# Optimization experiments

Hardware: AMD Instinct MI355X
Metric: run time of the kernel (lower is better)

## Reference

```python
import jax, jax.numpy as jnp
import numpy as np

INF = 100000000.0
TOPK = 27


def _box_iou(a, b):
    # a: [N,4] (x1,y1,x2,y2), b: [G,4] -> iou [N,G]
    area_a = (a[:, 2] - a[:, 0]) * (a[:, 3] - a[:, 1])
    area_b = (b[:, 2] - b[:, 0]) * (b[:, 3] - b[:, 1])
    lt = jnp.maximum(a[:, None, :2], b[None, :, :2])
    rb = jnp.minimum(a[:, None, 2:], b[None, :, 2:])
    wh = jnp.clip(rb - lt, 0.0)
    inter = wh[..., 0] * wh[..., 1]
    union = area_a[:, None] + area_b[None, :] - inter
    return inter / union, union


def _assign_one(anchors, gts, tokens):
    # anchors [N,4], gts [G,4], tokens [G,T]
    N = anchors.shape[0]
    G = gts.shape[0]
    ious, _ = _box_iou(anchors, gts)  # [N,G]

    a_cx = (anchors[:, 2] + anchors[:, 0]) * 0.5
    a_cy = (anchors[:, 3] + anchors[:, 1]) * 0.5
    g_cx = (gts[:, 2] + gts[:, 0]) * 0.5
    g_cy = (gts[:, 3] + gts[:, 1]) * 0.5

    # pairwise center distance [N,G]
    dist = jnp.sqrt((a_cx[:, None] - g_cx[None, :]) ** 2 +
                    (a_cy[:, None] - g_cy[None, :]) ** 2)

    # topk nearest anchors per gt (smallest distance) -> idxs [G,TOPK]
    _, topk_idxs = jax.lax.top_k(-dist.T, TOPK)

    # candidate ious [G,TOPK]
    cand = jnp.take_along_axis(ious.T, topk_idxs, axis=1)
    iou_mean = cand.mean(axis=1)
    iou_std = cand.std(axis=1, ddof=1)  # torch.std is unbiased
    is_pos = cand >= (iou_mean + iou_std)[:, None]

    # center-inside-gt check [G,TOPK]
    ax = a_cx[topk_idxs]
    ay = a_cy[topk_idxs]
    l = ax - gts[:, 0:1]
    t = ay - gts[:, 1:2]
    r = gts[:, 2:3] - ax
    b = gts[:, 3:4] - ay
    is_in_gts = jnp.minimum(jnp.minimum(l, t), jnp.minimum(r, b)) > 0.01
    is_pos = is_pos & is_in_gts

    # scatter candidate ious into flat [G*N] buffer of -INF (indices are unique)
    flat_idx = (jnp.arange(G)[:, None] * N + topk_idxs).reshape(-1)
    vals = ious.T.reshape(-1)[flat_idx]
    scat = jnp.where(is_pos.reshape(-1), vals, -INF)
    ious_inf = jnp.full((G * N,), -INF, dtype=ious.dtype).at[flat_idx].set(scat)
    ious_inf = ious_inf.reshape(G, N).T  # [N,G]

    anchors_to_gt_values = ious_inf.max(axis=1)          # [N]
    anchors_to_gt_indexs = ious_inf.argmax(axis=1)       # [N]

    matched_gts = gts[anchors_to_gt_indexs]              # [N,4]

    T = tokens.shape[1]
    unmatched = jnp.zeros((T,), tokens.dtype).at[-1].set(1.0)
    token_labels = jnp.where((anchors_to_gt_values == -INF)[:, None],
                             unmatched[None, :],
                             tokens[anchors_to_gt_indexs])  # [N,T]
    return anchors_to_gt_values, anchors_to_gt_indexs, matched_gts, token_labels


def setup_inputs() -> dict:
    key = jax.random.key(0)
    k1, k2, k3, k4, k5 = jax.random.split(key, 5)
    B, N, G, T = 8, 100000, 64, 256
    # anchors: valid x1<x2, y1<y2 boxes on a ~1024px canvas
    a_c = jax.random.uniform(k1, (B, N, 2), jnp.float32, 0.0, 1024.0)
    a_wh = jax.random.uniform(k2, (B, N, 2), jnp.float32, 8.0, 128.0)
    anchor_boxes = jnp.concatenate([a_c - a_wh / 2, a_c + a_wh / 2], axis=-1)
    g_c = jax.random.uniform(k3, (B, G, 2), jnp.float32, 0.0, 1024.0)
    g_wh = jax.random.uniform(k4, (B, G, 2), jnp.float32, 64.0, 512.0)
    gt_boxes = jnp.concatenate([g_c - g_wh / 2, g_c + g_wh / 2], axis=-1)
    token_map = jax.random.uniform(k5, (B, G, T), jnp.float32)
    return {"anchor_boxes": anchor_boxes, "gt_boxes": gt_boxes,
            "token_map": token_map}


def reference(anchor_boxes, gt_boxes, token_map):
    return jax.vmap(_assign_one)(anchor_boxes, gt_boxes, token_map)
```

## Files before the change

### kernel.cpp

```cpp
#include <hip/hip_runtime.h>
#include <cstdint>

constexpr int B = 8, N = 100000, G = 64, T = 256, TOPK = 27;
constexpr int BN = B * N;
constexpr int CAP = 2048;
#define NEG_INF_VAL (-100000000.0f)

__global__ __launch_bounds__(256) void atss_centers_kernel(
    const float* __restrict__ anchors, float2* __restrict__ ctr)
{
#pragma clang fp contract(off)
  int i = blockIdx.x * 256 + threadIdx.x;
  if (i < BN) {
    float4 ab = ((const float4*)anchors)[i];
    ctr[i] = make_float2((ab.z + ab.x) * 0.5f, (ab.w + ab.y) * 0.5f);
  }
}

__global__ __launch_bounds__(256) void atss_assign_kernel(
    const float* __restrict__ anchors,
    const float2* __restrict__ ctr,
    const float* __restrict__ gts,
    unsigned long long* __restrict__ best)
{
#pragma clang fp contract(off)
  __shared__ float s_d[CAP];
  __shared__ int   s_i[CAP];
  __shared__ int   s_cnt;
  __shared__ int   s_sel[TOPK];
  __shared__ float s_iou[TOPK];
  __shared__ int   s_in[TOPK];
  __shared__ float s_thresh;

  const int bg  = blockIdx.x;
  const int b   = bg / G;
  const int g   = bg % G;
  const int tid = threadIdx.x;

  const float4 gbox = ((const float4*)gts)[bg];
  const float g_cx = (gbox.z + gbox.x) * 0.5f;
  const float g_cy = (gbox.w + gbox.y) * 0.5f;

  const float4*  abase = (const float4*)(anchors + (size_t)b * N * 4);
  const float2*  cbase = ctr + (size_t)b * N;

  float thr = 24.0f;
  int M = 0;
  for (int attempt = 0; attempt < 8; ++attempt) {
    if (tid == 0) s_cnt = 0;
    __syncthreads();
    for (int n = tid; n < N; n += 256) {
      float2 c = cbase[n];
      float dx = c.x - g_cx, dy = c.y - g_cy;
      float d = __fsqrt_rn(__fmul_rn(dx, dx) + __fmul_rn(dy, dy));
      if (d < thr) {
        int p = atomicAdd(&s_cnt, 1);
        if (p < CAP) { s_d[p] = d; s_i[p] = n; }
      }
    }
    __syncthreads();
    int cnt = s_cnt;
    __syncthreads();
    if (cnt >= TOPK && cnt <= CAP) { M = cnt; break; }
    thr = (cnt < TOPK) ? thr * 4.0f : thr * 0.5f;
  }

  for (int s = tid; s < M; s += 256) {
    unsigned long long pk_s =
        ((unsigned long long)__float_as_uint(s_d[s]) << 20) |
        (unsigned long long)(unsigned)s_i[s];
    int rank = 0;
    for (int j = 0; j < M; ++j) {
      unsigned long long pk_j =
          ((unsigned long long)__float_as_uint(s_d[j]) << 20) |
          (unsigned long long)(unsigned)s_i[j];
      rank += (pk_j < pk_s) ? 1 : 0;
    }
    if (rank < TOPK) s_sel[rank] = s_i[s];
  }
  __syncthreads();

  if (tid < TOPK) {
    int a = s_sel[tid];
    float4 ab = abase[a];
    float area_a = __fmul_rn(ab.z - ab.x, ab.w - ab.y);
    float area_b = __fmul_rn(gbox.z - gbox.x, gbox.w - gbox.y);
    float ltx = fmaxf(ab.x, gbox.x), lty = fmaxf(ab.y, gbox.y);
    float rbx = fminf(ab.z, gbox.z), rby = fminf(ab.w, gbox.w);
    float w = fmaxf(rbx - ltx, 0.0f), h = fmaxf(rby - lty, 0.0f);
    float inter = __fmul_rn(w, h);
    float uni = (area_a + area_b) - inter;
    s_iou[tid] = inter / uni;
    float acx = (ab.z + ab.x) * 0.5f, acy = (ab.w + ab.y) * 0.5f;
    float l = acx - gbox.x, t = acy - gbox.y;
    float r = gbox.z - acx, bt = gbox.w - acy;
    float mn = fminf(fminf(l, t), fminf(r, bt));
    s_in[tid] = (mn > 0.01f) ? 1 : 0;
  }
  __syncthreads();

  if (tid == 0) {
    float sum = 0.0f;
    for (int k = 0; k < TOPK; ++k) sum += s_iou[k];
    float mean = sum / (float)TOPK;
    float vs = 0.0f;
    for (int k = 0; k < TOPK; ++k) {
      float d = s_iou[k] - mean;
      vs += __fmul_rn(d, d);
    }
    float sd = __fsqrt_rn(vs / (float)(TOPK - 1));
    s_thresh = mean + sd;
  }
  __syncthreads();

  if (tid < TOPK) {
    float iou = s_iou[tid];
    if (s_in[tid] && iou >= s_thresh) {
      unsigned long long pk =
          ((unsigned long long)__float_as_uint(iou) << 32) |
          (unsigned long long)(0xFFFFFFFFu - (unsigned)g);
      atomicMax(&best[(size_t)b * N + s_sel[tid]], pk);
    }
  }
}

__global__ __launch_bounds__(256) void atss_write_kernel(
    const unsigned long long* __restrict__ best,
    const float* __restrict__ gts,
    const float* __restrict__ tokens,
    float* __restrict__ out)
{
  float* __restrict__ out_val = out;
  float* __restrict__ out_idx = out + (size_t)BN;
  float* __restrict__ out_mg  = out + (size_t)2 * BN;
  float* __restrict__ out_tok = out + (size_t)6 * BN;

  __shared__ int s_row[256];

  const int tid = threadIdx.x;
  const int i0  = blockIdx.x * 256;
  const int i   = i0 + tid;

  unsigned long long p = best[i];
  const int b_ = i / N;
  int g = 0;
  float val = NEG_INF_VAL;
  if (p != 0ULL) {
    g   = (int)(0xFFFFFFFFu - (unsigned)(p & 0xFFFFFFFFULL));
    val = __uint_as_float((unsigned)(p >> 32));
  }
  const int row = b_ * G + g;
  s_row[tid] = (p != 0ULL) ? row : -1;

  out_val[i] = val;
  out_idx[i] = (float)g;
  ((float4*)out_mg)[i] = ((const float4*)gts)[row];
  __syncthreads();

  const int lane = tid & 63;
  const int sub  = tid >> 6;
  const float4* tok4 = (const float4*)tokens;
#pragma unroll 4
  for (int s = 0; s < 64; ++s) {
    int a = (s << 2) + sub;
    int r = s_row[a];
    float4 t;
    if (r >= 0) {
      t = tok4[(size_t)r * 64 + lane];
    } else {
      t = make_float4(0.0f, 0.0f, 0.0f, 0.0f);
      if (lane == 63) t.w = 1.0f;
    }
    ((float4*)(out_tok + (size_t)(i0 + a) * T))[lane] = t;
  }
}

extern "C" void kernel_launch(void* const* d_in, const int* in_sizes, int n_in,
                              void* d_out, int out_size, void* d_ws, size_t ws_size,
                              hipStream_t stream) {
  const float* anchors = (const float*)d_in[0];
  const float* gts     = (const float*)d_in[1];
  const float* tokens  = (const float*)d_in[2];
  float* out = (float*)d_out;

  unsigned long long* best = (unsigned long long*)d_ws;
  float2* ctr = (float2*)((char*)d_ws + sizeof(unsigned long long) * (size_t)BN);

  hipMemsetAsync(best, 0, sizeof(unsigned long long) * (size_t)BN, stream);
  atss_centers_kernel<<<(BN + 255) / 256, 256, 0, stream>>>(anchors, ctr);
  atss_assign_kernel<<<B * G, 256, 0, stream>>>(anchors, ctr, gts, best);
  atss_write_kernel<<<BN / 256, 256, 0, stream>>>(best, gts, tokens, out);
}
```

Measured before the change: 960.1 us.

## Zero token output with memset and sparsely write only matched anchors' tokens

The 800K x 256 token output is now cleared with a bulk memset, and the write kernel only writes the trailing 1.0 for unmatched anchors and copies token rows for matched anchors, which are compacted in shared memory. The zeroing of the best array moves into the centers kernel, replacing its separate memset. This aims to cut per-thread store work in the write kernel, since most anchors are unmatched. The full 800 MB buffer is still written once by the memset, so the gain rests on memset bandwidth beating the kernel's store loop, and the scattered single-float writes add some overhead.

```diff
diff --git a/kernel.cpp b/kernel.cpp
--- a/kernel.cpp
+++ b/kernel.cpp
@@ -6,12 +6,14 @@
 constexpr int CAP = 2048;
 #define NEG_INF_VAL (-100000000.0f)
 
-__global__ __launch_bounds__(256) void atss_centers_kernel(
-    const float* __restrict__ anchors, float2* __restrict__ ctr)
+__global__ __launch_bounds__(256) void atss_prep_kernel(
+    const float* __restrict__ anchors, float2* __restrict__ ctr,
+    unsigned long long* __restrict__ best)
 {
 #pragma clang fp contract(off)
   int i = blockIdx.x * 256 + threadIdx.x;
   if (i < BN) {
+    best[i] = 0ULL;
     float4 ab = ((const float4*)anchors)[i];
     ctr[i] = make_float2((ab.z + ab.x) * 0.5f, (ab.w + ab.y) * 0.5f);
   }
@@ -124,7 +126,7 @@
   }
 }
 
-__global__ __launch_bounds__(256) void atss_write_kernel(
+__global__ __launch_bounds__(256) void atss_sparse_write_kernel(
     const unsigned long long* __restrict__ best,
     const float* __restrict__ gts,
     const float* __restrict__ tokens,
@@ -135,11 +137,16 @@
   float* __restrict__ out_mg  = out + (size_t)2 * BN;
   float* __restrict__ out_tok = out + (size_t)6 * BN;
 
-  __shared__ int s_row[256];
+  __shared__ int s_m_anchor[256];
+  __shared__ int s_m_row[256];
+  __shared__ int s_m_cnt;
 
   const int tid = threadIdx.x;
   const int i0  = blockIdx.x * 256;
   const int i   = i0 + tid;
+
+  if (tid == 0) s_m_cnt = 0;
+  __syncthreads();
 
   unsigned long long p = best[i];
   const int b_ = i / N;
@@ -150,28 +157,28 @@
     val = __uint_as_float((unsigned)(p >> 32));
   }
   const int row = b_ * G + g;
-  s_row[tid] = (p != 0ULL) ? row : -1;
 
   out_val[i] = val;
   out_idx[i] = (float)g;
   ((float4*)out_mg)[i] = ((const float4*)gts)[row];
+
+  if (p != 0ULL) {
+    int s = atomicAdd(&s_m_cnt, 1);
+    s_m_anchor[s] = i;
+    s_m_row[s]    = row;
+  } else {
+    out_tok[(size_t)i * T + (T - 1)] = 1.0f;
+  }
   __syncthreads();
 
   const int lane = tid & 63;
-  const int sub  = tid >> 6;
+  const int wv   = tid >> 6;
+  const int cnt  = s_m_cnt;
   const float4* tok4 = (const float4*)tokens;
-#pragma unroll 4
-  for (int s = 0; s < 64; ++s) {
-    int a = (s << 2) + sub;
-    int r = s_row[a];
-    float4 t;
-    if (r >= 0) {
-      t = tok4[(size_t)r * 64 + lane];
-    } else {
-      t = make_float4(0.0f, 0.0f, 0.0f, 0.0f);
-      if (lane == 63) t.w = 1.0f;
-    }
-    ((float4*)(out_tok + (size_t)(i0 + a) * T))[lane] = t;
+  for (int s = wv; s < cnt; s += 4) {
+    const int a = s_m_anchor[s];
+    const int r = s_m_row[s];
+    ((float4*)(out_tok + (size_t)a * T))[lane] = tok4[(size_t)r * 64 + lane];
   }
 }
 
@@ -186,8 +193,9 @@
   unsigned long long* best = (unsigned long long*)d_ws;
   float2* ctr = (float2*)((char*)d_ws + sizeof(unsigned long long) * (size_t)BN);
 
-  hipMemsetAsync(best, 0, sizeof(unsigned long long) * (size_t)BN, stream);
-  atss_centers_kernel<<<(BN + 255) / 256, 256, 0, stream>>>(anchors, ctr);
+  hipMemsetAsync(out + (size_t)6 * BN, 0, sizeof(float) * (size_t)BN * T, stream);
+
+  atss_prep_kernel<<<(BN + 255) / 256, 256, 0, stream>>>(anchors, ctr, best);
   atss_assign_kernel<<<B * G, 256, 0, stream>>>(anchors, ctr, gts, best);
-  atss_write_kernel<<<BN / 256, 256, 0, stream>>>(best, gts, tokens, out);
-}
+  atss_sparse_write_kernel<<<BN / 256, 256, 0, stream>>>(best, gts, tokens, out);
+}
```

Measured after the change: 998.3 us. +4.0%, slower.

## Fold best-init into prep kernel and split token write into persistent-wave kernel

Applied to the files above, without the earlier changes.

Drops the memset by zeroing the best buffer inside the centers kernel. The write kernel is split into a small post kernel that writes values, indices and matched boxes and stores row ids to a workspace buffer. A separate token kernel then has each wave stream a contiguous range of output rows with one float4 per lane. The aim is fewer launches and a token copy that streams better, at the cost of an extra launch and an extra pass over the row buffer.

```diff
diff --git a/kernel.cpp b/kernel.cpp
--- a/kernel.cpp
+++ b/kernel.cpp
@@ -6,12 +6,14 @@
 constexpr int CAP = 2048;
 #define NEG_INF_VAL (-100000000.0f)
 
-__global__ __launch_bounds__(256) void atss_centers_kernel(
-    const float* __restrict__ anchors, float2* __restrict__ ctr)
+__global__ __launch_bounds__(256) void atss_prep_kernel(
+    const float* __restrict__ anchors, float2* __restrict__ ctr,
+    unsigned long long* __restrict__ best)
 {
 #pragma clang fp contract(off)
   int i = blockIdx.x * 256 + threadIdx.x;
   if (i < BN) {
+    best[i] = 0ULL;
     float4 ab = ((const float4*)anchors)[i];
     ctr[i] = make_float2((ab.z + ab.x) * 0.5f, (ab.w + ab.y) * 0.5f);
   }
@@ -124,23 +126,13 @@
   }
 }
 
-__global__ __launch_bounds__(256) void atss_write_kernel(
+__global__ __launch_bounds__(256) void atss_post_kernel(
     const unsigned long long* __restrict__ best,
     const float* __restrict__ gts,
-    const float* __restrict__ tokens,
-    float* __restrict__ out)
+    float* __restrict__ out,
+    int* __restrict__ rowbuf)
 {
-  float* __restrict__ out_val = out;
-  float* __restrict__ out_idx = out + (size_t)BN;
-  float* __restrict__ out_mg  = out + (size_t)2 * BN;
-  float* __restrict__ out_tok = out + (size_t)6 * BN;
-
-  __shared__ int s_row[256];
-
-  const int tid = threadIdx.x;
-  const int i0  = blockIdx.x * 256;
-  const int i   = i0 + tid;
-
+  const int i = blockIdx.x * 256 + threadIdx.x;
   unsigned long long p = best[i];
   const int b_ = i / N;
   int g = 0;
@@ -150,28 +142,38 @@
     val = __uint_as_float((unsigned)(p >> 32));
   }
   const int row = b_ * G + g;
-  s_row[tid] = (p != 0ULL) ? row : -1;
 
-  out_val[i] = val;
-  out_idx[i] = (float)g;
-  ((float4*)out_mg)[i] = ((const float4*)gts)[row];
-  __syncthreads();
+  out[i] = val;
+  out[(size_t)BN + i] = (float)g;
+  ((float4*)(out + (size_t)2 * BN))[i] = ((const float4*)gts)[row];
+  rowbuf[i] = (p != 0ULL) ? row : -1;
+}
 
-  const int lane = tid & 63;
-  const int sub  = tid >> 6;
+constexpr int TW_BLOCKS = 2048;
+constexpr int ROWS_PER_WAVE = (BN + 8191) / 8192;
+
+__global__ __launch_bounds__(256) void atss_tok_kernel(
+    const int* __restrict__ rowbuf,
+    const float* __restrict__ tokens,
+    float* __restrict__ out_tok)
+{
+  const int wv   = (blockIdx.x * 256 + threadIdx.x) >> 6;
+  const int lane = threadIdx.x & 63;
   const float4* tok4 = (const float4*)tokens;
-#pragma unroll 4
-  for (int s = 0; s < 64; ++s) {
-    int a = (s << 2) + sub;
-    int r = s_row[a];
+  float4* o4 = (float4*)out_tok;
+
+  const int r0 = wv * ROWS_PER_WAVE;
+  const int r1 = (r0 + ROWS_PER_WAVE < BN) ? r0 + ROWS_PER_WAVE : BN;
+#pragma unroll 2
+  for (int row = r0; row < r1; ++row) {
+    int r = rowbuf[row];
     float4 t;
     if (r >= 0) {
       t = tok4[(size_t)r * 64 + lane];
     } else {
-      t = make_float4(0.0f, 0.0f, 0.0f, 0.0f);
-      if (lane == 63) t.w = 1.0f;
+      t = make_float4(0.0f, 0.0f, 0.0f, (lane == 63) ? 1.0f : 0.0f);
     }
-    ((float4*)(out_tok + (size_t)(i0 + a) * T))[lane] = t;
+    o4[(size_t)row * 64 + lane] = t;
   }
 }
 
@@ -185,9 +187,10 @@
 
   unsigned long long* best = (unsigned long long*)d_ws;
   float2* ctr = (float2*)((char*)d_ws + sizeof(unsigned long long) * (size_t)BN);
+  int* rowbuf = (int*)((char*)d_ws + (sizeof(unsigned long long) + sizeof(float2)) * (size_t)BN);
 
-  hipMemsetAsync(best, 0, sizeof(unsigned long long) * (size_t)BN, stream);
-  atss_centers_kernel<<<(BN + 255) / 256, 256, 0, stream>>>(anchors, ctr);
+  atss_prep_kernel<<<(BN + 255) / 256, 256, 0, stream>>>(anchors, ctr, best);
   atss_assign_kernel<<<B * G, 256, 0, stream>>>(anchors, ctr, gts, best);
-  atss_write_kernel<<<BN / 256, 256, 0, stream>>>(best, gts, tokens, out);
+  atss_post_kernel<<<BN / 256, 256, 0, stream>>>(best, gts, out, rowbuf);
+  atss_tok_kernel<<<TW_BLOCKS, 256, 0, stream>>>(rowbuf, tokens, out + (size_t)6 * BN);
 }
```

After: 979.7 us. +2.0%, slower.
